# Optimization experiments

Measured on AMD Instinct MI355X. Metric: run time of the kernel, lower is better.

Reference implementation:

```python
import jax, jax.numpy as jnp
import numpy as np

N_NODES = 65536
N_EDGES = 1048576
D_FEAT = 64
K_HOPS = 10
ALPHA = 0.1


def setup_inputs() -> dict:
    key = jax.random.key(0)
    k1, k2 = jax.random.split(key, 2)
    x = jax.random.normal(k1, (N_NODES, D_FEAT), dtype=jnp.float32)
    edge_index = jax.random.randint(k2, (2, N_EDGES), 0, N_NODES, dtype=jnp.int32)
    # PPR init of the learnable polynomial coefficients (length K+1)
    temp = ALPHA * (1.0 - ALPHA) ** np.arange(K_HOPS + 1)
    temp[-1] = (1.0 - ALPHA) ** K_HOPS
    temp = jnp.asarray(temp, dtype=jnp.float32)
    return {"x": x, "temp": temp, "edge_index": edge_index}


def reference(x, temp, edge_index):
    # GCN-normalized adjacency with self-loops (gcn_norm, homophily=True path):
    #   A_hat = D^{-1/2} (A + I) D^{-1/2}
    N = x.shape[0]
    K = temp.shape[0] - 1
    loops = jnp.arange(N, dtype=edge_index.dtype)
    src = jnp.concatenate([edge_index[0], loops])  # message sources (x_j)
    dst = jnp.concatenate([edge_index[1], loops])  # aggregation targets
    ones = jnp.ones(src.shape[0], dtype=x.dtype)
    deg = jax.ops.segment_sum(ones, dst, num_segments=N)  # self-loops => deg > 0
    dinv = jax.lax.rsqrt(deg)
    norm = dinv[src] * dinv[dst]  # [E+N]

    # hidden = temp[K-1]*x; then K-1 propagation hops accumulating temp[k]*A_hat^m x
    hidden = temp[K - 1] * x
    h = x
    for k in range(K - 2, -1, -1):
        # sparse propagate: scatter-add of norm-weighted gathered source features
        h = jax.ops.segment_sum(norm[:, None] * h[src], dst, num_segments=N)
        hidden = hidden + temp[k] * h
    return hidden
```

## Files before the change

### kernel.cpp

```cpp
#include <hip/hip_runtime.h>
#include <hip/hip_fp16.h>

#define N_NODES 65536
#define N_EDGES 1048576
#define D_FEAT  64
#define BUCKET  64

typedef float vfloat4 __attribute__((ext_vector_type(4)));


__global__ void count_deg(const int* __restrict__ dst, int* __restrict__ counts,
                          int* __restrict__ rank) {
    int e = blockIdx.x * blockDim.x + threadIdx.x;
    if (e < N_EDGES) rank[e] = atomicAdd(&counts[dst[e]], 1);
}

__global__ void compute_dinv(const int* __restrict__ counts, float* __restrict__ dinv) {
    int v = blockIdx.x * blockDim.x + threadIdx.x;
    if (v < N_NODES) dinv[v] = rsqrtf((float)(counts[v] + 1));
}

__global__ void scatter_src(const int* __restrict__ src, const int* __restrict__ dst,
                            const int* __restrict__ rank, int* __restrict__ csr_src) {
    int e = blockIdx.x * blockDim.x + threadIdx.x;
    if (e >= N_EDGES) return;
    csr_src[dst[e] * BUCKET + rank[e]] = src[e];
}

__global__ void cvt_x(const float* __restrict__ x, const float* __restrict__ dinv,
                      __half* __restrict__ t0) {
    int i = blockIdx.x * blockDim.x + threadIdx.x;
    int v = i >> 4;
    float dv = dinv[v];
    float4 val = ((const float4*)x)[i];
    __half2 lo = __floats2half2_rn(dv * val.x, dv * val.y);
    __half2 hi = __floats2half2_rn(dv * val.z, dv * val.w);
    unsigned long long o = ((unsigned long long)(*(const unsigned int*)&hi) << 32)
                         | (*(const unsigned int*)&lo);
    ((unsigned long long*)t0)[i] = o;
}

__global__ void __launch_bounds__(256) hop_kernel(
        const __half* __restrict__ tab, const float* __restrict__ x,
        __half* __restrict__ tab_out, float* __restrict__ out_f32,
        const float* __restrict__ temp, const int* __restrict__ counts,
        const int* __restrict__ csr_src, const float* __restrict__ dinv, int k) {
    int gtid = blockIdx.x * blockDim.x + threadIdx.x;
    int wave = __builtin_amdgcn_readfirstlane(gtid >> 6);
    int lane = gtid & 63;
    int q = lane >> 4;
    int f = lane & 15;

    int v0 = wave * 4;
    float tk = temp[k];
    float sc = (k == 1) ? temp[0] : 1.0f;

    int   cnt[4];
    float dv[4];
    #pragma unroll
    for (int j = 0; j < 4; ++j) {
        cnt[j] = counts[v0 + j];
        dv[j]  = dinv[v0 + j];
    }
    int maxc = max(max(cnt[0], cnt[1]), max(cnt[2], cnt[3]));
    int iters = (maxc + 15) >> 4;

    const unsigned long long* t2 = (const unsigned long long*)tab;
    float a0[4] = {0.f, 0.f, 0.f, 0.f};
    float a1[4] = {0.f, 0.f, 0.f, 0.f};
    float a2[4] = {0.f, 0.f, 0.f, 0.f};
    float a3[4] = {0.f, 0.f, 0.f, 0.f};

    for (int r = 0; r < iters; ++r) {
        int e0 = r * 16;
        #pragma unroll
        for (int j = 0; j < 4; ++j) {
            const int4* bj = (const int4*)(csr_src + (v0 + j) * BUCKET + e0);
            #pragma unroll
            for (int g = 0; g < 4; ++g) {
                int4 sg = bj[g];
                int s01 = (q & 1) ? sg.y : sg.x;
                int s23 = (q & 1) ? sg.w : sg.z;
                int s   = (q & 2) ? s23 : s01;
                bool ok = (e0 + 4 * g + q) < cnt[j];
                unsigned long long row = t2[s * 16 + f];
                unsigned int rl = (unsigned int)row, rh = (unsigned int)(row >> 32);
                float2 lo = __half22float2(*(const __half2*)&rl);
                float2 hi = __half22float2(*(const __half2*)&rh);
                a0[j] += ok ? lo.x : 0.0f;
                a1[j] += ok ? lo.y : 0.0f;
                a2[j] += ok ? hi.x : 0.0f;
                a3[j] += ok ? hi.y : 0.0f;
            }
        }
    }

    #pragma unroll
    for (int j = 0; j < 4; ++j) {
        a0[j] += __shfl_xor(a0[j], 16); a0[j] += __shfl_xor(a0[j], 32);
        a1[j] += __shfl_xor(a1[j], 16); a1[j] += __shfl_xor(a1[j], 32);
        a2[j] += __shfl_xor(a2[j], 16); a2[j] += __shfl_xor(a2[j], 32);
        a3[j] += __shfl_xor(a3[j], 16); a3[j] += __shfl_xor(a3[j], 32);
    }

    #pragma unroll
    for (int j = 0; j < 4; ++j) {
        int v = v0 + j;
        vfloat4 xv = ((const vfloat4*)x)[v * 16 + f];
        unsigned long long srow = t2[v * 16 + f];
        unsigned int sl = (unsigned int)srow, sh = (unsigned int)(srow >> 32);
        float2 slo = __half22float2(*(const __half2*)&sl);
        float2 shi = __half22float2(*(const __half2*)&sh);
        float m = sc * dv[j];
        float r0 = m * (a0[j] + slo.x) + tk * xv.x;
        float r1 = m * (a1[j] + slo.y) + tk * xv.y;
        float r2 = m * (a2[j] + shi.x) + tk * xv.z;
        float r3 = m * (a3[j] + shi.y) + tk * xv.w;
        if (q == 0) {
            if (k == 9) {
                vfloat4 o = {r0, r1, r2, r3};
                ((vfloat4*)out_f32)[v * 16 + f] = o;
            } else {
                float d2 = dv[j];
                __half2 lo = __floats2half2_rn(d2 * r0, d2 * r1);
                __half2 hi = __floats2half2_rn(d2 * r2, d2 * r3);
                unsigned long long o =
                    ((unsigned long long)(*(const unsigned int*)&hi) << 32)
                    | (*(const unsigned int*)&lo);
                ((unsigned long long*)tab_out)[v * 16 + f] = o;
            }
        }
    }
}

extern "C" void kernel_launch(void* const* d_in, const int* in_sizes, int n_in,
                              void* d_out, int out_size, void* d_ws, size_t ws_size,
                              hipStream_t stream) {
    const float* x    = (const float*)d_in[0];
    const float* temp = (const float*)d_in[1];
    const int*   ei   = (const int*)d_in[2];
    const int* src = ei;
    const int* dst = ei + N_EDGES;
    float* out = (float*)d_out;

    char* ws = (char*)d_ws;
    int*    counts  = (int*)   (ws + 0x000000);
    float*  dinv    = (float*) (ws + 0x040000);
    int*    rank    = (int*)   (ws + 0x080000);
    int*    csr_src = (int*)   (ws + 0x500000);
    __half* tA      = (__half*)(ws + 0x1500000);
    __half* tB      = (__half*)(ws + 0x1D00000);

    (void)hipMemsetAsync(counts, 0, N_NODES * sizeof(int), stream);
    (void)hipMemsetAsync(csr_src, 0, N_NODES * BUCKET * sizeof(int), stream);

    count_deg<<<N_EDGES / 256, 256, 0, stream>>>(dst, counts, rank);
    compute_dinv<<<N_NODES / 256, 256, 0, stream>>>(counts, dinv);
    scatter_src<<<N_EDGES / 256, 256, 0, stream>>>(src, dst, rank, csr_src);
    cvt_x<<<(N_NODES * 16) / 256, 256, 0, stream>>>(x, dinv, tA);

    const int hop_blocks = (N_NODES / 4) * 64 / 256;
    const __half* gin = tA;
    for (int k = 1; k <= 9; ++k) {
        __half* gout = (k & 1) ? tB : tA;
        hop_kernel<<<hop_blocks, 256, 0, stream>>>(gin, x, gout, out, temp,
                                                   counts, csr_src, dinv, k);
        gin = gout;
    }
}
```

Before: 382.8 us.

## Sort nodes by degree and shrink neighbor loop granularity to four edges

Builds a degree-bucketed permutation with a histogram, a scan and an atomic placement pass, so each wave handles four nodes of similar degree. The hop loop now advances four edges per iteration instead of sixteen, which cuts masked-out gathers when a wave's nodes have unequal degrees. In exchange it adds three small setup kernels and an indirect node lookup, and output rows are written in a scattered order. Iteration count now tracks the exact maximum degree within the wave.

```diff
diff --git a/kernel.cpp b/kernel.cpp
--- a/kernel.cpp
+++ b/kernel.cpp
@@ -5,6 +5,7 @@
 #define N_EDGES 1048576
 #define D_FEAT  64
 #define BUCKET  64
+#define DEGBINS 64
 
 typedef float vfloat4 __attribute__((ext_vector_type(4)));
 
@@ -18,6 +19,35 @@
 __global__ void compute_dinv(const int* __restrict__ counts, float* __restrict__ dinv) {
     int v = blockIdx.x * blockDim.x + threadIdx.x;
     if (v < N_NODES) dinv[v] = rsqrtf((float)(counts[v] + 1));
+}
+
+__global__ void hist_deg(const int* __restrict__ counts, int* __restrict__ hist) {
+    int v = blockIdx.x * blockDim.x + threadIdx.x;
+    int d = min(counts[v], DEGBINS - 1);
+    atomicAdd(&hist[d], 1);
+}
+
+__global__ void scan_hist(const int* __restrict__ hist, int* __restrict__ cur) {
+    __shared__ int s[DEGBINS];
+    int t = threadIdx.x;
+    int v = hist[t];
+    s[t] = v;
+    __syncthreads();
+    for (int o = 1; o < DEGBINS; o <<= 1) {
+        int u = (t >= o) ? s[t - o] : 0;
+        __syncthreads();
+        s[t] += u;
+        __syncthreads();
+    }
+    cur[t] = s[t] - v;
+}
+
+__global__ void make_perm(const int* __restrict__ counts, int* __restrict__ cur,
+                          int* __restrict__ perm) {
+    int v = blockIdx.x * blockDim.x + threadIdx.x;
+    int d = min(counts[v], DEGBINS - 1);
+    int pos = atomicAdd(&cur[d], 1);
+    perm[pos] = v;
 }
 
 __global__ void scatter_src(const int* __restrict__ src, const int* __restrict__ dst,
@@ -44,26 +74,28 @@
         const __half* __restrict__ tab, const float* __restrict__ x,
         __half* __restrict__ tab_out, float* __restrict__ out_f32,
         const float* __restrict__ temp, const int* __restrict__ counts,
-        const int* __restrict__ csr_src, const float* __restrict__ dinv, int k) {
+        const int* __restrict__ csr_src, const float* __restrict__ dinv,
+        const int* __restrict__ perm, int k) {
     int gtid = blockIdx.x * blockDim.x + threadIdx.x;
     int wave = __builtin_amdgcn_readfirstlane(gtid >> 6);
     int lane = gtid & 63;
     int q = lane >> 4;
     int f = lane & 15;
 
-    int v0 = wave * 4;
     float tk = temp[k];
     float sc = (k == 1) ? temp[0] : 1.0f;
 
+    int4 pv = *(const int4*)(perm + wave * 4);
+    int vids[4] = {pv.x, pv.y, pv.z, pv.w};
     int   cnt[4];
     float dv[4];
     #pragma unroll
     for (int j = 0; j < 4; ++j) {
-        cnt[j] = counts[v0 + j];
-        dv[j]  = dinv[v0 + j];
+        cnt[j] = counts[vids[j]];
+        dv[j]  = dinv[vids[j]];
     }
     int maxc = max(max(cnt[0], cnt[1]), max(cnt[2], cnt[3]));
-    int iters = (maxc + 15) >> 4;
+    int iters = (maxc + 3) >> 2;
 
     const unsigned long long* t2 = (const unsigned long long*)tab;
     float a0[4] = {0.f, 0.f, 0.f, 0.f};
@@ -71,27 +103,24 @@
     float a2[4] = {0.f, 0.f, 0.f, 0.f};
     float a3[4] = {0.f, 0.f, 0.f, 0.f};
 
+    #pragma unroll 4
     for (int r = 0; r < iters; ++r) {
-        int e0 = r * 16;
+        int e0 = r * 4;
         #pragma unroll
         for (int j = 0; j < 4; ++j) {
-            const int4* bj = (const int4*)(csr_src + (v0 + j) * BUCKET + e0);
-            #pragma unroll
-            for (int g = 0; g < 4; ++g) {
-                int4 sg = bj[g];
-                int s01 = (q & 1) ? sg.y : sg.x;
-                int s23 = (q & 1) ? sg.w : sg.z;
-                int s   = (q & 2) ? s23 : s01;
-                bool ok = (e0 + 4 * g + q) < cnt[j];
-                unsigned long long row = t2[s * 16 + f];
-                unsigned int rl = (unsigned int)row, rh = (unsigned int)(row >> 32);
-                float2 lo = __half22float2(*(const __half2*)&rl);
-                float2 hi = __half22float2(*(const __half2*)&rh);
-                a0[j] += ok ? lo.x : 0.0f;
-                a1[j] += ok ? lo.y : 0.0f;
-                a2[j] += ok ? hi.x : 0.0f;
-                a3[j] += ok ? hi.y : 0.0f;
-            }
+            int4 sg = *(const int4*)(csr_src + vids[j] * BUCKET + e0);
+            int s01 = (q & 1) ? sg.y : sg.x;
+            int s23 = (q & 1) ? sg.w : sg.z;
+            int s   = (q & 2) ? s23 : s01;
+            bool ok = (e0 + q) < cnt[j];
+            unsigned long long row = t2[s * 16 + f];
+            unsigned int rl = (unsigned int)row, rh = (unsigned int)(row >> 32);
+            float2 lo = __half22float2(*(const __half2*)&rl);
+            float2 hi = __half22float2(*(const __half2*)&rh);
+            a0[j] += ok ? lo.x : 0.0f;
+            a1[j] += ok ? lo.y : 0.0f;
+            a2[j] += ok ? hi.x : 0.0f;
+            a3[j] += ok ? hi.y : 0.0f;
         }
     }
 
@@ -105,7 +134,7 @@
 
     #pragma unroll
     for (int j = 0; j < 4; ++j) {
-        int v = v0 + j;
+        int v = vids[j];
         vfloat4 xv = ((const vfloat4*)x)[v * 16 + f];
         unsigned long long srow = t2[v * 16 + f];
         unsigned int sl = (unsigned int)srow, sh = (unsigned int)(srow >> 32);
@@ -147,15 +176,22 @@
     int*    counts  = (int*)   (ws + 0x000000);
     float*  dinv    = (float*) (ws + 0x040000);
     int*    rank    = (int*)   (ws + 0x080000);
+    int*    perm    = (int*)   (ws + 0x480000);
+    int*    hist    = (int*)   (ws + 0x4C0000);
+    int*    cur     = (int*)   (ws + 0x4C0400);
     int*    csr_src = (int*)   (ws + 0x500000);
     __half* tA      = (__half*)(ws + 0x1500000);
     __half* tB      = (__half*)(ws + 0x1D00000);
 
     (void)hipMemsetAsync(counts, 0, N_NODES * sizeof(int), stream);
+    (void)hipMemsetAsync(hist, 0, DEGBINS * sizeof(int), stream);
     (void)hipMemsetAsync(csr_src, 0, N_NODES * BUCKET * sizeof(int), stream);
 
     count_deg<<<N_EDGES / 256, 256, 0, stream>>>(dst, counts, rank);
     compute_dinv<<<N_NODES / 256, 256, 0, stream>>>(counts, dinv);
+    hist_deg<<<N_NODES / 256, 256, 0, stream>>>(counts, hist);
+    scan_hist<<<1, DEGBINS, 0, stream>>>(hist, cur);
+    make_perm<<<N_NODES / 256, 256, 0, stream>>>(counts, cur, perm);
     scatter_src<<<N_EDGES / 256, 256, 0, stream>>>(src, dst, rank, csr_src);
     cvt_x<<<(N_NODES * 16) / 256, 256, 0, stream>>>(x, dinv, tA);
 
@@ -164,7 +200,7 @@
     for (int k = 1; k <= 9; ++k) {
         __half* gout = (k & 1) ? tB : tA;
         hop_kernel<<<hop_blocks, 256, 0, stream>>>(gin, x, gout, out, temp,
-                                                   counts, csr_src, dinv, k);
+                                                   counts, csr_src, dinv, perm, k);
         gin = gout;
     }
 }
```

Measured after the change: 737.9 us. +92.7%, slower.

## Split feature table into halves, use 16-bit CSR indices, fuse degree count and scatter

Applied to the files above, without the earlier changes.

Splits the fp16 feature table into two 32-feature halves stored separately. Each hop block handles one half for 16 nodes, with blocks interleaved so the working set of each half-table is smaller and more cache-resident. CSR source indices become 16-bit, and the degree count and CSR scatter are fused into one kernel with 4 edges per thread. x is also pre-converted to fp16 for the epilogue. The 16-bit indices rely on N_NODES being at most 65536, and the fp16 x adds some rounding in the temp[k]*x term.

```diff
diff --git a/kernel.cpp b/kernel.cpp
--- a/kernel.cpp
+++ b/kernel.cpp
@@ -3,16 +3,24 @@
 
 #define N_NODES 65536
 #define N_EDGES 1048576
-#define D_FEAT  64
 #define BUCKET  64
 
 typedef float vfloat4 __attribute__((ext_vector_type(4)));
+typedef unsigned long long ull;
 
 
-__global__ void count_deg(const int* __restrict__ dst, int* __restrict__ counts,
-                          int* __restrict__ rank) {
-    int e = blockIdx.x * blockDim.x + threadIdx.x;
-    if (e < N_EDGES) rank[e] = atomicAdd(&counts[dst[e]], 1);
+__global__ void fused_scatter(const int* __restrict__ src, const int* __restrict__ dst,
+                              int* __restrict__ counts, unsigned short* __restrict__ csr) {
+    int t = blockIdx.x * blockDim.x + threadIdx.x;
+    const int stride = N_EDGES / 4;
+    #pragma unroll
+    for (int i = 0; i < 4; ++i) {
+        int e = t + i * stride;
+        int s = src[e];
+        int d = dst[e];
+        int r = atomicAdd(&counts[d], 1);
+        csr[d * BUCKET + r] = (unsigned short)s;
+    }
 }
 
 __global__ void compute_dinv(const int* __restrict__ counts, float* __restrict__ dinv) {
@@ -20,114 +28,118 @@
     if (v < N_NODES) dinv[v] = rsqrtf((float)(counts[v] + 1));
 }
 
-__global__ void scatter_src(const int* __restrict__ src, const int* __restrict__ dst,
-                            const int* __restrict__ rank, int* __restrict__ csr_src) {
-    int e = blockIdx.x * blockDim.x + threadIdx.x;
-    if (e >= N_EDGES) return;
-    csr_src[dst[e] * BUCKET + rank[e]] = src[e];
-}
-
 __global__ void cvt_x(const float* __restrict__ x, const float* __restrict__ dinv,
-                      __half* __restrict__ t0) {
+                      __half* __restrict__ t0_lo, __half* __restrict__ t0_hi,
+                      __half* __restrict__ xh_lo, __half* __restrict__ xh_hi) {
     int i = blockIdx.x * blockDim.x + threadIdx.x;
     int v = i >> 4;
+    int f = i & 15;
     float dv = dinv[v];
     float4 val = ((const float4*)x)[i];
-    __half2 lo = __floats2half2_rn(dv * val.x, dv * val.y);
-    __half2 hi = __floats2half2_rn(dv * val.z, dv * val.w);
-    unsigned long long o = ((unsigned long long)(*(const unsigned int*)&hi) << 32)
-                         | (*(const unsigned int*)&lo);
-    ((unsigned long long*)t0)[i] = o;
+    __half2 xl = __floats2half2_rn(val.x, val.y);
+    __half2 xhh = __floats2half2_rn(val.z, val.w);
+    ull ox = ((ull)(*(const unsigned*)&xhh) << 32) | (*(const unsigned*)&xl);
+    __half2 tl = __floats2half2_rn(dv * val.x, dv * val.y);
+    __half2 th = __floats2half2_rn(dv * val.z, dv * val.w);
+    ull ot = ((ull)(*(const unsigned*)&th) << 32) | (*(const unsigned*)&tl);
+    if (f < 8) {
+        ((ull*)xh_lo)[v * 8 + f] = ox;
+        ((ull*)t0_lo)[v * 8 + f] = ot;
+    } else {
+        ((ull*)xh_hi)[v * 8 + (f - 8)] = ox;
+        ((ull*)t0_hi)[v * 8 + (f - 8)] = ot;
+    }
 }
 
 __global__ void __launch_bounds__(256) hop_kernel(
-        const __half* __restrict__ tab, const float* __restrict__ x,
-        __half* __restrict__ tab_out, float* __restrict__ out_f32,
-        const float* __restrict__ temp, const int* __restrict__ counts,
-        const int* __restrict__ csr_src, const float* __restrict__ dinv, int k) {
-    int gtid = blockIdx.x * blockDim.x + threadIdx.x;
-    int wave = __builtin_amdgcn_readfirstlane(gtid >> 6);
-    int lane = gtid & 63;
-    int q = lane >> 4;
-    int f = lane & 15;
+        const __half* __restrict__ tin_lo, __half* __restrict__ tout_lo,
+        const __half* __restrict__ tin_hi, __half* __restrict__ tout_hi,
+        const __half* __restrict__ xh_lo, const __half* __restrict__ xh_hi,
+        float* __restrict__ out_f32, const float* __restrict__ temp,
+        const int* __restrict__ counts, const unsigned short* __restrict__ csr,
+        const float* __restrict__ dinv, int k) {
+    int b = blockIdx.x;
+    int c = (b & 4) ? 1 : 0;
+    int l = ((b >> 3) << 2) | (b & 3);
+    int wv = threadIdx.x >> 6;
+    int v0 = __builtin_amdgcn_readfirstlane(l * 16 + wv * 4);
+    int lane = threadIdx.x & 63;
+    int q = lane >> 3;
+    int f = lane & 7;
 
-    int v0 = wave * 4;
+    const ull* t2 = (const ull*)(c ? tin_hi : tin_lo);
+    __half* tout = c ? tout_hi : tout_lo;
+    const ull* xh = (const ull*)(c ? xh_hi : xh_lo);
+
     float tk = temp[k];
     float sc = (k == 1) ? temp[0] : 1.0f;
 
-    int   cnt[4];
-    float dv[4];
-    #pragma unroll
-    for (int j = 0; j < 4; ++j) {
-        cnt[j] = counts[v0 + j];
-        dv[j]  = dinv[v0 + j];
-    }
+    int4 cv = *(const int4*)(counts + v0);
+    int cnt[4] = {cv.x, cv.y, cv.z, cv.w};
+    float4 dvv = *(const float4*)(dinv + v0);
+    float dv[4] = {dvv.x, dvv.y, dvv.z, dvv.w};
+
     int maxc = max(max(cnt[0], cnt[1]), max(cnt[2], cnt[3]));
-    int iters = (maxc + 15) >> 4;
+    int iters = (maxc + 7) >> 3;
 
-    const unsigned long long* t2 = (const unsigned long long*)tab;
     float a0[4] = {0.f, 0.f, 0.f, 0.f};
     float a1[4] = {0.f, 0.f, 0.f, 0.f};
     float a2[4] = {0.f, 0.f, 0.f, 0.f};
     float a3[4] = {0.f, 0.f, 0.f, 0.f};
 
+    #pragma unroll 2
     for (int r = 0; r < iters; ++r) {
-        int e0 = r * 16;
+        int e0 = r * 8;
         #pragma unroll
         for (int j = 0; j < 4; ++j) {
-            const int4* bj = (const int4*)(csr_src + (v0 + j) * BUCKET + e0);
-            #pragma unroll
-            for (int g = 0; g < 4; ++g) {
-                int4 sg = bj[g];
-                int s01 = (q & 1) ? sg.y : sg.x;
-                int s23 = (q & 1) ? sg.w : sg.z;
-                int s   = (q & 2) ? s23 : s01;
-                bool ok = (e0 + 4 * g + q) < cnt[j];
-                unsigned long long row = t2[s * 16 + f];
-                unsigned int rl = (unsigned int)row, rh = (unsigned int)(row >> 32);
-                float2 lo = __half22float2(*(const __half2*)&rl);
-                float2 hi = __half22float2(*(const __half2*)&rh);
-                a0[j] += ok ? lo.x : 0.0f;
-                a1[j] += ok ? lo.y : 0.0f;
-                a2[j] += ok ? hi.x : 0.0f;
-                a3[j] += ok ? hi.y : 0.0f;
-            }
+            int4 sg = *(const int4*)(csr + (v0 + j) * BUCKET + e0);
+            int sel1 = (q & 2) ? sg.y : sg.x;
+            int sel2 = (q & 2) ? sg.w : sg.z;
+            int word = (q & 4) ? sel2 : sel1;
+            int s = (word >> ((q & 1) * 16)) & 0xffff;
+            ull row = t2[s * 8 + f];
+            row = ((e0 + q) < cnt[j]) ? row : 0ull;
+            unsigned rl = (unsigned)row, rh = (unsigned)(row >> 32);
+            float2 lo = __half22float2(*(const __half2*)&rl);
+            float2 hi = __half22float2(*(const __half2*)&rh);
+            a0[j] += lo.x; a1[j] += lo.y; a2[j] += hi.x; a3[j] += hi.y;
         }
     }
 
     #pragma unroll
     for (int j = 0; j < 4; ++j) {
-        a0[j] += __shfl_xor(a0[j], 16); a0[j] += __shfl_xor(a0[j], 32);
-        a1[j] += __shfl_xor(a1[j], 16); a1[j] += __shfl_xor(a1[j], 32);
-        a2[j] += __shfl_xor(a2[j], 16); a2[j] += __shfl_xor(a2[j], 32);
-        a3[j] += __shfl_xor(a3[j], 16); a3[j] += __shfl_xor(a3[j], 32);
+        a0[j] += __shfl_xor(a0[j], 8); a0[j] += __shfl_xor(a0[j], 16); a0[j] += __shfl_xor(a0[j], 32);
+        a1[j] += __shfl_xor(a1[j], 8); a1[j] += __shfl_xor(a1[j], 16); a1[j] += __shfl_xor(a1[j], 32);
+        a2[j] += __shfl_xor(a2[j], 8); a2[j] += __shfl_xor(a2[j], 16); a2[j] += __shfl_xor(a2[j], 32);
+        a3[j] += __shfl_xor(a3[j], 8); a3[j] += __shfl_xor(a3[j], 16); a3[j] += __shfl_xor(a3[j], 32);
     }
 
     #pragma unroll
     for (int j = 0; j < 4; ++j) {
         int v = v0 + j;
-        vfloat4 xv = ((const vfloat4*)x)[v * 16 + f];
-        unsigned long long srow = t2[v * 16 + f];
-        unsigned int sl = (unsigned int)srow, sh = (unsigned int)(srow >> 32);
-        float2 slo = __half22float2(*(const __half2*)&sl);
-        float2 shi = __half22float2(*(const __half2*)&sh);
+        ull sx = xh[v * 8 + f];
+        ull st = t2[v * 8 + f];
+        unsigned sxl = (unsigned)sx, sxh = (unsigned)(sx >> 32);
+        unsigned stl = (unsigned)st, sth = (unsigned)(st >> 32);
+        float2 xlo = __half22float2(*(const __half2*)&sxl);
+        float2 xhi = __half22float2(*(const __half2*)&sxh);
+        float2 slo = __half22float2(*(const __half2*)&stl);
+        float2 shi = __half22float2(*(const __half2*)&sth);
         float m = sc * dv[j];
-        float r0 = m * (a0[j] + slo.x) + tk * xv.x;
-        float r1 = m * (a1[j] + slo.y) + tk * xv.y;
-        float r2 = m * (a2[j] + shi.x) + tk * xv.z;
-        float r3 = m * (a3[j] + shi.y) + tk * xv.w;
+        float r0 = m * (a0[j] + slo.x) + tk * xlo.x;
+        float r1 = m * (a1[j] + slo.y) + tk * xlo.y;
+        float r2 = m * (a2[j] + shi.x) + tk * xhi.x;
+        float r3 = m * (a3[j] + shi.y) + tk * xhi.y;
         if (q == 0) {
             if (k == 9) {
                 vfloat4 o = {r0, r1, r2, r3};
-                ((vfloat4*)out_f32)[v * 16 + f] = o;
+                ((vfloat4*)out_f32)[v * 16 + c * 8 + f] = o;
             } else {
                 float d2 = dv[j];
-                __half2 lo = __floats2half2_rn(d2 * r0, d2 * r1);
-                __half2 hi = __floats2half2_rn(d2 * r2, d2 * r3);
-                unsigned long long o =
-                    ((unsigned long long)(*(const unsigned int*)&hi) << 32)
-                    | (*(const unsigned int*)&lo);
-                ((unsigned long long*)tab_out)[v * 16 + f] = o;
+                __half2 plo = __floats2half2_rn(d2 * r0, d2 * r1);
+                __half2 phi = __floats2half2_rn(d2 * r2, d2 * r3);
+                ull o = ((ull)(*(const unsigned*)&phi) << 32) | (*(const unsigned*)&plo);
+                ((ull*)tout)[v * 8 + f] = o;
             }
         }
     }
@@ -144,27 +156,31 @@
     float* out = (float*)d_out;
 
     char* ws = (char*)d_ws;
-    int*    counts  = (int*)   (ws + 0x000000);
-    float*  dinv    = (float*) (ws + 0x040000);
-    int*    rank    = (int*)   (ws + 0x080000);
-    int*    csr_src = (int*)   (ws + 0x500000);
-    __half* tA      = (__half*)(ws + 0x1500000);
-    __half* tB      = (__half*)(ws + 0x1D00000);
+    int*            counts = (int*)            (ws + 0x000000);
+    float*          dinv   = (float*)          (ws + 0x040000);
+    unsigned short* csr    = (unsigned short*) (ws + 0x080000);
+    __half*         xh_lo  = (__half*)         (ws + 0x880000);
+    __half*         xh_hi  = (__half*)         (ws + 0xC80000);
+    __half*         tA_lo  = (__half*)         (ws + 0x1080000);
+    __half*         tB_lo  = (__half*)         (ws + 0x1480000);
+    __half*         tA_hi  = (__half*)         (ws + 0x1880000);
+    __half*         tB_hi  = (__half*)         (ws + 0x1C80000);
 
     (void)hipMemsetAsync(counts, 0, N_NODES * sizeof(int), stream);
-    (void)hipMemsetAsync(csr_src, 0, N_NODES * BUCKET * sizeof(int), stream);
+    (void)hipMemsetAsync(csr, 0, N_NODES * BUCKET * sizeof(unsigned short), stream);
 
-    count_deg<<<N_EDGES / 256, 256, 0, stream>>>(dst, counts, rank);
+    fused_scatter<<<(N_EDGES / 4) / 256, 256, 0, stream>>>(src, dst, counts, csr);
     compute_dinv<<<N_NODES / 256, 256, 0, stream>>>(counts, dinv);
-    scatter_src<<<N_EDGES / 256, 256, 0, stream>>>(src, dst, rank, csr_src);
-    cvt_x<<<(N_NODES * 16) / 256, 256, 0, stream>>>(x, dinv, tA);
+    cvt_x<<<(N_NODES * 16) / 256, 256, 0, stream>>>(x, dinv, tA_lo, tA_hi, xh_lo, xh_hi);
 
-    const int hop_blocks = (N_NODES / 4) * 64 / 256;
-    const __half* gin = tA;
+    const int hop_blocks = 8192;
     for (int k = 1; k <= 9; ++k) {
-        __half* gout = (k & 1) ? tB : tA;
-        hop_kernel<<<hop_blocks, 256, 0, stream>>>(gin, x, gout, out, temp,
-                                                   counts, csr_src, dinv, k);
-        gin = gout;
+        const __half* gi_lo = (k & 1) ? tA_lo : tB_lo;
+        __half*       go_lo = (k & 1) ? tB_lo : tA_lo;
+        const __half* gi_hi = (k & 1) ? tA_hi : tB_hi;
+        __half*       go_hi = (k & 1) ? tB_hi : tA_hi;
+        hop_kernel<<<hop_blocks, 256, 0, stream>>>(gi_lo, go_lo, gi_hi, go_hi,
+                                                   xh_lo, xh_hi, out, temp,
+                                                   counts, csr, dinv, k);
     }
 }
```

After: 455.0 us. +18.8%, slower.

## Compress CSR indices to 16-bit and keep an fp16 copy of x

Applied to the files above, without the earlier changes.

Stores the CSR neighbour lists as unsigned short instead of int, which halves the index bytes each hop reads (the 16-bit index relies on N_NODES being 65536). Adds an fp16 copy of x, built in cvt_x and read in the hop epilogue instead of fp32 x. Also loads counts and dinv with single vector loads and masks gathered rows before accumulating. This trades lower precision in the tk*x term for less memory traffic per hop.

```diff
diff --git a/kernel.cpp b/kernel.cpp
--- a/kernel.cpp
+++ b/kernel.cpp
@@ -3,10 +3,10 @@
 
 #define N_NODES 65536
 #define N_EDGES 1048576
-#define D_FEAT  64
 #define BUCKET  64
 
 typedef float vfloat4 __attribute__((ext_vector_type(4)));
+typedef unsigned long long ull;
 
 
 __global__ void count_deg(const int* __restrict__ dst, int* __restrict__ counts,
@@ -21,30 +21,35 @@
 }
 
 __global__ void scatter_src(const int* __restrict__ src, const int* __restrict__ dst,
-                            const int* __restrict__ rank, int* __restrict__ csr_src) {
+                            const int* __restrict__ rank,
+                            unsigned short* __restrict__ csr) {
     int e = blockIdx.x * blockDim.x + threadIdx.x;
     if (e >= N_EDGES) return;
-    csr_src[dst[e] * BUCKET + rank[e]] = src[e];
+    csr[dst[e] * BUCKET + rank[e]] = (unsigned short)src[e];
 }
 
 __global__ void cvt_x(const float* __restrict__ x, const float* __restrict__ dinv,
-                      __half* __restrict__ t0) {
+                      __half* __restrict__ t0, __half* __restrict__ xh) {
     int i = blockIdx.x * blockDim.x + threadIdx.x;
     int v = i >> 4;
     float dv = dinv[v];
     float4 val = ((const float4*)x)[i];
-    __half2 lo = __floats2half2_rn(dv * val.x, dv * val.y);
-    __half2 hi = __floats2half2_rn(dv * val.z, dv * val.w);
-    unsigned long long o = ((unsigned long long)(*(const unsigned int*)&hi) << 32)
-                         | (*(const unsigned int*)&lo);
-    ((unsigned long long*)t0)[i] = o;
+    __half2 xl = __floats2half2_rn(val.x, val.y);
+    __half2 xh2 = __floats2half2_rn(val.z, val.w);
+    ull ox = ((ull)(*(const unsigned*)&xh2) << 32) | (*(const unsigned*)&xl);
+    __half2 tl = __floats2half2_rn(dv * val.x, dv * val.y);
+    __half2 th = __floats2half2_rn(dv * val.z, dv * val.w);
+    ull ot = ((ull)(*(const unsigned*)&th) << 32) | (*(const unsigned*)&tl);
+    ((ull*)xh)[i] = ox;
+    ((ull*)t0)[i] = ot;
 }
 
 __global__ void __launch_bounds__(256) hop_kernel(
-        const __half* __restrict__ tab, const float* __restrict__ x,
+        const __half* __restrict__ tab, const __half* __restrict__ xh,
         __half* __restrict__ tab_out, float* __restrict__ out_f32,
         const float* __restrict__ temp, const int* __restrict__ counts,
-        const int* __restrict__ csr_src, const float* __restrict__ dinv, int k) {
+        const unsigned short* __restrict__ csr, const float* __restrict__ dinv,
+        int k) {
     int gtid = blockIdx.x * blockDim.x + threadIdx.x;
     int wave = __builtin_amdgcn_readfirstlane(gtid >> 6);
     int lane = gtid & 63;
@@ -55,17 +60,15 @@
     float tk = temp[k];
     float sc = (k == 1) ? temp[0] : 1.0f;
 
-    int   cnt[4];
-    float dv[4];
-    #pragma unroll
-    for (int j = 0; j < 4; ++j) {
-        cnt[j] = counts[v0 + j];
-        dv[j]  = dinv[v0 + j];
-    }
+    int4 cv = *(const int4*)(counts + v0);
+    int cnt[4] = {cv.x, cv.y, cv.z, cv.w};
+    float4 dvv = *(const float4*)(dinv + v0);
+    float dv[4] = {dvv.x, dvv.y, dvv.z, dvv.w};
+
     int maxc = max(max(cnt[0], cnt[1]), max(cnt[2], cnt[3]));
     int iters = (maxc + 15) >> 4;
 
-    const unsigned long long* t2 = (const unsigned long long*)tab;
+    const ull* t2 = (const ull*)tab;
     float a0[4] = {0.f, 0.f, 0.f, 0.f};
     float a1[4] = {0.f, 0.f, 0.f, 0.f};
     float a2[4] = {0.f, 0.f, 0.f, 0.f};
@@ -75,22 +78,21 @@
         int e0 = r * 16;
         #pragma unroll
         for (int j = 0; j < 4; ++j) {
-            const int4* bj = (const int4*)(csr_src + (v0 + j) * BUCKET + e0);
+            const int4* bp = (const int4*)(csr + (v0 + j) * BUCKET + e0);
+            int4 sgA = bp[0];
+            int4 sgB = bp[1];
             #pragma unroll
             for (int g = 0; g < 4; ++g) {
-                int4 sg = bj[g];
-                int s01 = (q & 1) ? sg.y : sg.x;
-                int s23 = (q & 1) ? sg.w : sg.z;
-                int s   = (q & 2) ? s23 : s01;
-                bool ok = (e0 + 4 * g + q) < cnt[j];
-                unsigned long long row = t2[s * 16 + f];
-                unsigned int rl = (unsigned int)row, rh = (unsigned int)(row >> 32);
+                int4 sg = (g & 2) ? sgB : sgA;
+                int word = (g & 1) ? ((q & 2) ? sg.w : sg.z)
+                                   : ((q & 2) ? sg.y : sg.x);
+                int s = (word >> ((q & 1) * 16)) & 0xffff;
+                ull row = t2[s * 16 + f];
+                row = ((e0 + 4 * g + q) < cnt[j]) ? row : 0ull;
+                unsigned rl = (unsigned)row, rh = (unsigned)(row >> 32);
                 float2 lo = __half22float2(*(const __half2*)&rl);
                 float2 hi = __half22float2(*(const __half2*)&rh);
-                a0[j] += ok ? lo.x : 0.0f;
-                a1[j] += ok ? lo.y : 0.0f;
-                a2[j] += ok ? hi.x : 0.0f;
-                a3[j] += ok ? hi.y : 0.0f;
+                a0[j] += lo.x; a1[j] += lo.y; a2[j] += hi.x; a3[j] += hi.y;
             }
         }
     }
@@ -106,28 +108,30 @@
     #pragma unroll
     for (int j = 0; j < 4; ++j) {
         int v = v0 + j;
-        vfloat4 xv = ((const vfloat4*)x)[v * 16 + f];
-        unsigned long long srow = t2[v * 16 + f];
-        unsigned int sl = (unsigned int)srow, sh = (unsigned int)(srow >> 32);
-        float2 slo = __half22float2(*(const __half2*)&sl);
-        float2 shi = __half22float2(*(const __half2*)&sh);
+        ull sx = ((const ull*)xh)[v * 16 + f];
+        ull st = t2[v * 16 + f];
+        unsigned sxl = (unsigned)sx, sxh2 = (unsigned)(sx >> 32);
+        unsigned stl = (unsigned)st, sth = (unsigned)(st >> 32);
+        float2 xlo = __half22float2(*(const __half2*)&sxl);
+        float2 xhi = __half22float2(*(const __half2*)&sxh2);
+        float2 slo = __half22float2(*(const __half2*)&stl);
+        float2 shi = __half22float2(*(const __half2*)&sth);
         float m = sc * dv[j];
-        float r0 = m * (a0[j] + slo.x) + tk * xv.x;
-        float r1 = m * (a1[j] + slo.y) + tk * xv.y;
-        float r2 = m * (a2[j] + shi.x) + tk * xv.z;
-        float r3 = m * (a3[j] + shi.y) + tk * xv.w;
+        float r0 = m * (a0[j] + slo.x) + tk * xlo.x;
+        float r1 = m * (a1[j] + slo.y) + tk * xlo.y;
+        float r2 = m * (a2[j] + shi.x) + tk * xhi.x;
+        float r3 = m * (a3[j] + shi.y) + tk * xhi.y;
         if (q == 0) {
             if (k == 9) {
                 vfloat4 o = {r0, r1, r2, r3};
                 ((vfloat4*)out_f32)[v * 16 + f] = o;
             } else {
                 float d2 = dv[j];
-                __half2 lo = __floats2half2_rn(d2 * r0, d2 * r1);
-                __half2 hi = __floats2half2_rn(d2 * r2, d2 * r3);
-                unsigned long long o =
-                    ((unsigned long long)(*(const unsigned int*)&hi) << 32)
-                    | (*(const unsigned int*)&lo);
-                ((unsigned long long*)tab_out)[v * 16 + f] = o;
+                __half2 plo = __floats2half2_rn(d2 * r0, d2 * r1);
+                __half2 phi = __floats2half2_rn(d2 * r2, d2 * r3);
+                ull o = ((ull)(*(const unsigned*)&phi) << 32)
+                      | (*(const unsigned*)&plo);
+                ((ull*)tab_out)[v * 16 + f] = o;
             }
         }
     }
@@ -144,27 +148,28 @@
     float* out = (float*)d_out;
 
     char* ws = (char*)d_ws;
-    int*    counts  = (int*)   (ws + 0x000000);
-    float*  dinv    = (float*) (ws + 0x040000);
-    int*    rank    = (int*)   (ws + 0x080000);
-    int*    csr_src = (int*)   (ws + 0x500000);
-    __half* tA      = (__half*)(ws + 0x1500000);
-    __half* tB      = (__half*)(ws + 0x1D00000);
+    int*            counts = (int*)            (ws + 0x000000);
+    float*          dinv   = (float*)          (ws + 0x040000);
+    int*            rank   = (int*)            (ws + 0x080000);
+    unsigned short* csr    = (unsigned short*) (ws + 0x480000);
+    __half*         xh     = (__half*)         (ws + 0xC80000);
+    __half*         tA     = (__half*)         (ws + 0x1480000);
+    __half*         tB     = (__half*)         (ws + 0x1C80000);
 
     (void)hipMemsetAsync(counts, 0, N_NODES * sizeof(int), stream);
-    (void)hipMemsetAsync(csr_src, 0, N_NODES * BUCKET * sizeof(int), stream);
+    (void)hipMemsetAsync(csr, 0, N_NODES * BUCKET * sizeof(unsigned short), stream);
 
     count_deg<<<N_EDGES / 256, 256, 0, stream>>>(dst, counts, rank);
     compute_dinv<<<N_NODES / 256, 256, 0, stream>>>(counts, dinv);
-    scatter_src<<<N_EDGES / 256, 256, 0, stream>>>(src, dst, rank, csr_src);
-    cvt_x<<<(N_NODES * 16) / 256, 256, 0, stream>>>(x, dinv, tA);
+    scatter_src<<<N_EDGES / 256, 256, 0, stream>>>(src, dst, rank, csr);
+    cvt_x<<<(N_NODES * 16) / 256, 256, 0, stream>>>(x, dinv, tA, xh);
 
     const int hop_blocks = (N_NODES / 4) * 64 / 256;
     const __half* gin = tA;
     for (int k = 1; k <= 9; ++k) {
         __half* gout = (k & 1) ? tB : tA;
-        hop_kernel<<<hop_blocks, 256, 0, stream>>>(gin, x, gout, out, temp,
-                                                   counts, csr_src, dinv, k);
+        hop_kernel<<<hop_blocks, 256, 0, stream>>>(gin, xh, gout, out, temp,
+                                                   counts, csr, dinv, k);
         gin = gout;
     }
 }
```

Result: faster. 360.4 us (-5.9%).
